# Kernel optimization log

Hardware: AMD Instinct MI355X
Metric: run time of the kernel (lower is better)

The kernel has to match this reference:

```python
import jax, jax.numpy as jnp
import numpy as np

N, E, D, DFF, OUT = 50000, 800000, 128, 256, 119
NUM_MASK = 7500

def setup_inputs() -> dict:
    key = jax.random.key(0)
    ks = jax.random.split(key, 12)
    return {
        "x": jax.random.normal(ks[0], (N, D), jnp.float32),
        "edge_index": jax.random.randint(ks[1], (2, E), 0, N, jnp.int64),
        "edge_attr": jax.random.randint(ks[2], (E, 2), 0, 3, jnp.int64),
        "masked_idx": jax.random.randint(ks[3], (NUM_MASK,), 0, N, jnp.int64),
        "prelu_a": jnp.float32(0.25),
        "W_enc": jax.random.normal(ks[4], (D, D), jnp.float32) * (1.0 / np.sqrt(D)),
        "emb1": jax.random.normal(ks[5], (6, D), jnp.float32) * 0.1,
        "emb2": jax.random.normal(ks[6], (3, D), jnp.float32) * 0.1,
        "W1": jax.random.normal(ks[7], (DFF, D), jnp.float32) * (1.0 / np.sqrt(D)),
        "b1": jnp.zeros((DFF,), jnp.float32),
        "W2": jax.random.normal(ks[8], (OUT, DFF), jnp.float32) * (1.0 / np.sqrt(DFF)),
        "b2": jnp.zeros((OUT,), jnp.float32),
    }

def reference(x, edge_index, edge_attr, masked_idx, prelu_a, W_enc, emb1, emb2, W1, b1, W2, b2):
    n = x.shape[0]
    # PReLU -> enc_to_dec (no bias) -> zero masked nodes
    h = jnp.where(x > 0, x, prelu_a * x)
    h = h @ W_enc.T
    h = h.at[masked_idx].set(0.0)
    # add self loops (self-loop edge_attr = [4, 0])
    loop = jnp.arange(n, dtype=edge_index.dtype)
    src = jnp.concatenate([edge_index[0], loop])
    dst = jnp.concatenate([edge_index[1], loop])
    et = jnp.concatenate([edge_attr[:, 0], jnp.full((n,), 4, edge_attr.dtype)])
    ed = jnp.concatenate([edge_attr[:, 1], jnp.zeros((n,), edge_attr.dtype)])
    edge_emb = emb1[et] + emb2[ed]          # [E+N, D]
    msg = h[src] + edge_emb                 # gather + add
    aggr = jax.ops.segment_sum(msg, dst, num_segments=n)  # scatter-add
    # GIN MLP update
    hid = jax.nn.relu(aggr @ W1.T + b1)
    return hid @ W2.T + b2
```

## Files before the change

### kernel.cpp

```cpp
#include <hip/hip_runtime.h>
#include <hip/hip_fp16.h>


typedef unsigned long long ull;
typedef _Float16 half8 __attribute__((ext_vector_type(8)));
typedef float    f32x4 __attribute__((ext_vector_type(4)));

#define MFMA16(a, b, c) __builtin_amdgcn_mfma_f32_16x16x32_f16(a, b, c, 0, 0, 0)
#define BCAP 4608
#define EPB  2048

__global__ __launch_bounds__(256) void k_wconv(const float* __restrict__ Wen,
                                               const float* __restrict__ W1,
                                               const float* __restrict__ W2,
                                               __half* __restrict__ Wen16,
                                               __half* __restrict__ W1_16,
                                               __half* __restrict__ W2_16p,
                                               int* __restrict__ gcur)
{
    int i = blockIdx.x * 256 + threadIdx.x;
    if (blockIdx.x == 0) gcur[threadIdx.x] = 0;
    if (i < 128 * 128) Wen16[i] = __float2half(Wen[i]);
    if (i < 256 * 128) W1_16[i] = __float2half(W1[i]);
    if (i < 128 * 256) {
        int r = i >> 8;
        W2_16p[i] = (r < 119) ? __float2half(W2[i]) : __half(0.0f);
    }
}

__device__ __forceinline__ half8 prelu_h8(const float* __restrict__ p, float a)
{
    float4 v0 = *(const float4*)p;
    float4 v1 = *(const float4*)(p + 4);
    half8 r;
    r[0] = (_Float16)(v0.x > 0.f ? v0.x : a * v0.x);
    r[1] = (_Float16)(v0.y > 0.f ? v0.y : a * v0.y);
    r[2] = (_Float16)(v0.z > 0.f ? v0.z : a * v0.z);
    r[3] = (_Float16)(v0.w > 0.f ? v0.w : a * v0.w);
    r[4] = (_Float16)(v1.x > 0.f ? v1.x : a * v1.x);
    r[5] = (_Float16)(v1.y > 0.f ? v1.y : a * v1.y);
    r[6] = (_Float16)(v1.z > 0.f ? v1.z : a * v1.z);
    r[7] = (_Float16)(v1.w > 0.f ? v1.w : a * v1.w);
    return r;
}

__global__ __launch_bounds__(256) void k_pre(const float* __restrict__ x,
                                             const __half* __restrict__ Wen16,
                                             const float* __restrict__ prelu_a,
                                             __half* __restrict__ h16,
                                             const int* __restrict__ ei,
                                             const int* __restrict__ ea,
                                             int* __restrict__ gcur,
                                             unsigned int* __restrict__ binned,
                                             int n, int E, int nbEnc, int nbBin)
{
    __shared__ __half Wel[128 * 136];
    __shared__ int lcnt[256];
    int t = threadIdx.x;

    if ((int)blockIdx.x >= nbEnc) {
        int b = blockIdx.x - nbEnc;
        int e0 = b * EPB;
        lcnt[t] = 0;
        __syncthreads();
        unsigned int rec[8];
        int bk[8];
#pragma unroll
        for (int u = 0; u < 8; ++u) {
            int e = e0 + u * 256 + t;
            if (e < E) {
                int src = ei[e];
                int dst = ei[E + e];
                int et  = ea[2 * e];
                int ed  = ea[2 * e + 1];
                rec[u] = (unsigned int)src | ((unsigned int)et << 17)
                       | ((unsigned int)ed << 19)
                       | ((unsigned int)(dst & 255) << 21);
                bk[u] = dst >> 8;
                atomicAdd(&lcnt[bk[u]], 1);
            } else bk[u] = -1;
        }
        __syncthreads();
        int c = lcnt[t];
        lcnt[t] = (c > 0) ? atomicAdd(&gcur[t], c) : 0;
        __syncthreads();
#pragma unroll
        for (int u = 0; u < 8; ++u) {
            if (bk[u] >= 0) {
                int pos = atomicAdd(&lcnt[bk[u]], 1);
                if (pos < BCAP) binned[(size_t)bk[u] * BCAP + pos] = rec[u];
            }
        }
        return;
    }

    for (int c = t; c < 2048; c += 256) {
        int row = c >> 4, slot = c & 15;
        *(uint4*)((char*)Wel + row * 272 + slot * 16) =
            *(const uint4*)((const char*)Wen16 + (size_t)c * 16);
    }
    __syncthreads();
    int lane = t & 63, wid = t >> 6;
    int rowbase = blockIdx.x * 128 + wid * 32;
    int mr0 = min(rowbase + (lane & 15), n - 1);
    int mr1 = min(rowbase + 16 + (lane & 15), n - 1);
    int kg = (lane >> 4) * 8, slotb = lane >> 4;
    float a = prelu_a[0];
    f32x4 acc[16] = {};
#pragma unroll
    for (int ks = 0; ks < 4; ++ks) {
        half8 a0 = prelu_h8(x + ((size_t)mr0 << 7) + ks * 32 + kg, a);
        half8 a1 = prelu_h8(x + ((size_t)mr1 << 7) + ks * 32 + kg, a);
        const char* wp = (const char*)Wel + (size_t)(lane & 15) * 272
                       + (ks * 4 + slotb) * 16;
#pragma unroll
        for (int ct = 0; ct < 8; ++ct) {
            half8 bf = *(const half8*)(wp + ct * (16 * 272));
            acc[ct * 2]     = MFMA16(a0, bf, acc[ct * 2]);
            acc[ct * 2 + 1] = MFMA16(a1, bf, acc[ct * 2 + 1]);
        }
    }
#pragma unroll
    for (int ct = 0; ct < 8; ++ct)
#pragma unroll
        for (int h = 0; h < 2; ++h)
#pragma unroll
            for (int r = 0; r < 4; ++r) {
                int node = rowbase + h * 16 + ((lane >> 4) << 2) + r;
                if (node < n)
                    h16[((size_t)node << 7) + (ct << 4) + (lane & 15)] =
                        __float2half(acc[ct * 2 + h][r]);
            }
}

__global__ void k_mask(const int* __restrict__ midx,
                       unsigned int* __restrict__ h16u, int nm)
{
    int idx = blockIdx.x * blockDim.x + threadIdx.x;
    if (idx >= nm * 64) return;
    int m = idx >> 6, l = idx & 63;
    h16u[(((size_t)midx[m]) << 6) + l] = 0u;
}

__global__ __launch_bounds__(256) void k_bucket(const unsigned int* __restrict__ binned,
                                                const int* __restrict__ gcur,
                                                ull* __restrict__ cnt64,
                                                int* __restrict__ off,
                                                int* __restrict__ sorted,
                                                int n, int nb)
{
    __shared__ ull lc[256];
    __shared__ int sg[2][256];
    __shared__ int curs[256];
    int b = blockIdx.x, t = threadIdx.x;

    int gv = (t < nb) ? min(gcur[t], BCAP) : 0;
    sg[0][t] = gv;
    lc[t] = 0;
    __syncthreads();
    int cb = 0;
    for (int d = 1; d < 256; d <<= 1) {
        int v = sg[cb][t];
        if (t >= d) v += sg[cb][t - d];
        sg[cb ^ 1][t] = v;
        cb ^= 1;
        __syncthreads();
    }
    int ebase = (b == 0) ? 0 : sg[cb][b - 1];
    int mcnt = min(gcur[b], BCAP);
    __syncthreads();

    const unsigned int* bp = binned + (size_t)b * BCAP;
    for (int i = t; i < mcnt; i += 256) {
        unsigned int rec = bp[i];
        int dl = (rec >> 21) & 255;
        int et = (rec >> 17) & 3;
        int ed = (rec >> 19) & 3;
        atomicAdd(&lc[dl], (1ULL << (10 * et)) | (1ULL << (30 + 10 * ed)));
    }
    __syncthreads();

    ull c = lc[t];
    int deg = (int)((c & 1023) + ((c >> 10) & 1023) + ((c >> 20) & 1023));
    sg[0][t] = deg;
    __syncthreads();
    cb = 0;
    for (int d = 1; d < 256; d <<= 1) {
        int v = sg[cb][t];
        if (t >= d) v += sg[cb][t - d];
        sg[cb ^ 1][t] = v;
        cb ^= 1;
        __syncthreads();
    }
    int loc = sg[cb][t] - deg;
    int dst = (b << 8) + t;
    if (dst < n) {
        cnt64[dst] = c;
        off[dst]   = ebase + loc;
    }
    curs[t] = ebase + loc;
    __syncthreads();

    for (int i = t; i < mcnt; i += 256) {
        unsigned int rec = bp[i];
        int dl = (rec >> 21) & 255;
        int p = atomicAdd(&curs[dl], 1);
        sorted[p] = (int)(rec & 0x1FFFF);
    }
}

__global__ __launch_bounds__(256) void k_agg(const unsigned int* __restrict__ h16u,
                                             const int* __restrict__ off,
                                             const ull* __restrict__ cnt64,
                                             const int* __restrict__ sorted,
                                             const float* __restrict__ emb1,
                                             const float* __restrict__ emb2,
                                             unsigned int* __restrict__ aggr16u,
                                             int n)
{
    int lane = threadIdx.x & 63;
    int node = blockIdx.x * 4 + (threadIdx.x >> 6);
    if (node >= n) return;
    int p = lane << 1;
    float2 e10 = *(const float2*)(emb1 + 0 * 128 + p);
    float2 e11 = *(const float2*)(emb1 + 1 * 128 + p);
    float2 e12 = *(const float2*)(emb1 + 2 * 128 + p);
    float2 e14 = *(const float2*)(emb1 + 4 * 128 + p);
    float2 e20 = *(const float2*)(emb2 + 0 * 128 + p);
    float2 e21 = *(const float2*)(emb2 + 1 * 128 + p);
    float2 e22 = *(const float2*)(emb2 + 2 * 128 + p);

    ull c = cnt64[node];
    float c0 = (float)(c & 1023), c1 = (float)((c >> 10) & 1023),
          c2 = (float)((c >> 20) & 1023);
    float d0 = (float)((c >> 30) & 1023), d1 = (float)((c >> 40) & 1023),
          d2 = (float)((c >> 50) & 1023);
    int deg = (int)(c & 1023) + (int)((c >> 10) & 1023) + (int)((c >> 20) & 1023);

    unsigned int hv = h16u[(((size_t)node) << 6) + lane];
    float2 hf = __half22float2(*(__half2*)&hv);
    float2 acc, s1, s2, s3;
    s1 = s2 = s3 = make_float2(0.f, 0.f);
    acc.x = hf.x + e14.x + e20.x;
    acc.y = hf.y + e14.y + e20.y;
    acc.x = fmaf(c0, e10.x, fmaf(c1, e11.x, fmaf(c2, e12.x, acc.x)));
    acc.y = fmaf(c0, e10.y, fmaf(c1, e11.y, fmaf(c2, e12.y, acc.y)));
    acc.x = fmaf(d0, e20.x, fmaf(d1, e21.x, fmaf(d2, e22.x, acc.x)));
    acc.y = fmaf(d0, e20.y, fmaf(d1, e21.y, fmaf(d2, e22.y, acc.y)));

    int i = off[node], e = i + deg;
    for (; i + 3 < e; i += 4) {
        int a0 = sorted[i],     a1 = sorted[i + 1];
        int a2 = sorted[i + 2], a3 = sorted[i + 3];
        unsigned int v0 = h16u[(((size_t)a0) << 6) + lane];
        unsigned int v1 = h16u[(((size_t)a1) << 6) + lane];
        unsigned int v2 = h16u[(((size_t)a2) << 6) + lane];
        unsigned int v3 = h16u[(((size_t)a3) << 6) + lane];
        float2 f0 = __half22float2(*(__half2*)&v0);
        float2 f1 = __half22float2(*(__half2*)&v1);
        float2 f2 = __half22float2(*(__half2*)&v2);
        float2 f3 = __half22float2(*(__half2*)&v3);
        acc.x += f0.x; acc.y += f0.y;
        s1.x  += f1.x; s1.y  += f1.y;
        s2.x  += f2.x; s2.y  += f2.y;
        s3.x  += f3.x; s3.y  += f3.y;
    }
    for (; i < e; ++i) {
        unsigned int v0 = h16u[(((size_t)sorted[i]) << 6) + lane];
        float2 f0 = __half22float2(*(__half2*)&v0);
        acc.x += f0.x; acc.y += f0.y;
    }
    acc.x += s1.x + s2.x + s3.x;
    acc.y += s1.y + s2.y + s3.y;
    __half2 o = __floats2half2_rn(acc.x, acc.y);
    aggr16u[(size_t)node * 64 + lane] = *(unsigned int*)&o;
}

__global__ __launch_bounds__(256, 2) void k_mlp1(const __half* __restrict__ aggr16,
                                                 const __half* __restrict__ W1_16,
                                                 const float* __restrict__ b1,
                                                 __half* __restrict__ hid16, int n)
{
    __shared__ __half Wl[256 * 136];
    int t = threadIdx.x;
    for (int c = t; c < 4096; c += 256) {
        int row = c >> 4, slot = c & 15;
        *(uint4*)((char*)Wl + row * 272 + slot * 16) =
            *(const uint4*)((const char*)W1_16 + (size_t)c * 16);
    }
    __syncthreads();
    int lane = t & 63, wid = t >> 6;
    int rowbase = blockIdx.x * 128 + wid * 32;
    int mr0 = min(rowbase + (lane & 15), n - 1);
    int mr1 = min(rowbase + 16 + (lane & 15), n - 1);
    int kg = (lane >> 4) * 8, slotb = lane >> 4;
    f32x4 acc[32] = {};
#pragma unroll
    for (int ks = 0; ks < 4; ++ks) {
        half8 a0 = *(const half8*)(aggr16 + ((size_t)mr0 << 7) + ks * 32 + kg);
        half8 a1 = *(const half8*)(aggr16 + ((size_t)mr1 << 7) + ks * 32 + kg);
        const char* wp = (const char*)Wl + (size_t)(lane & 15) * 272
                       + (ks * 4 + slotb) * 16;
#pragma unroll
        for (int ct = 0; ct < 16; ++ct) {
            half8 bf = *(const half8*)(wp + ct * (16 * 272));
            acc[ct * 2]     = MFMA16(a0, bf, acc[ct * 2]);
            acc[ct * 2 + 1] = MFMA16(a1, bf, acc[ct * 2 + 1]);
        }
    }
#pragma unroll
    for (int ct = 0; ct < 16; ++ct) {
        int col = (ct << 4) + (lane & 15);
        float bb = b1[col];
#pragma unroll
        for (int h = 0; h < 2; ++h)
#pragma unroll
            for (int r = 0; r < 4; ++r) {
                int node = rowbase + h * 16 + ((lane >> 4) << 2) + r;
                if (node < n) {
                    float v = acc[ct * 2 + h][r] + bb;
                    hid16[((size_t)node << 8) + col] =
                        __float2half(v > 0.f ? v : 0.f);
                }
            }
    }
}

__global__ __launch_bounds__(256) void k_mlp2(const __half* __restrict__ hid16,
                                              const __half* __restrict__ W2_16p,
                                              const float* __restrict__ b2,
                                              float* __restrict__ out, int n)
{
    __shared__ __half W2l[128 * 264];
    int t = threadIdx.x;
    for (int c = t; c < 4096; c += 256) {
        int row = c >> 5, slot = c & 31;
        *(uint4*)((char*)W2l + row * 528 + slot * 16) =
            *(const uint4*)((const char*)W2_16p + (size_t)c * 16);
    }
    __syncthreads();
    int lane = t & 63, wid = t >> 6;
    int rowbase = blockIdx.x * 128 + wid * 32;
    int mr0 = min(rowbase + (lane & 15), n - 1);
    int mr1 = min(rowbase + 16 + (lane & 15), n - 1);
    int kg = (lane >> 4) * 8, slotb = lane >> 4;
    f32x4 acc[16] = {};
#pragma unroll
    for (int ks = 0; ks < 8; ++ks) {
        half8 a0 = *(const half8*)(hid16 + ((size_t)mr0 << 8) + ks * 32 + kg);
        half8 a1 = *(const half8*)(hid16 + ((size_t)mr1 << 8) + ks * 32 + kg);
        const char* wp = (const char*)W2l + (size_t)(lane & 15) * 528
                       + (ks * 4 + slotb) * 16;
#pragma unroll
        for (int ct = 0; ct < 8; ++ct) {
            half8 bf = *(const half8*)(wp + ct * (16 * 528));
            acc[ct * 2]     = MFMA16(a0, bf, acc[ct * 2]);
            acc[ct * 2 + 1] = MFMA16(a1, bf, acc[ct * 2 + 1]);
        }
    }
#pragma unroll
    for (int ct = 0; ct < 8; ++ct) {
        int col = (ct << 4) + (lane & 15);
        if (col >= 119) continue;
        float bb = b2[col];
#pragma unroll
        for (int h = 0; h < 2; ++h)
#pragma unroll
            for (int r = 0; r < 4; ++r) {
                int node = rowbase + h * 16 + ((lane >> 4) << 2) + r;
                if (node < n)
                    out[(size_t)node * 119 + col] = acc[ct * 2 + h][r] + bb;
            }
    }
}

extern "C" void kernel_launch(void* const* d_in, const int* in_sizes, int n_in,
                              void* d_out, int out_size, void* d_ws, size_t ws_size,
                              hipStream_t stream)
{
    const float* x    = (const float*)d_in[0];
    const int*   ei   = (const int*)d_in[1];
    const int*   ea   = (const int*)d_in[2];
    const int*   midx = (const int*)d_in[3];
    const float* pa   = (const float*)d_in[4];
    const float* Wen  = (const float*)d_in[5];
    const float* emb1 = (const float*)d_in[6];
    const float* emb2 = (const float*)d_in[7];
    const float* W1   = (const float*)d_in[8];
    const float* b1   = (const float*)d_in[9];
    const float* W2   = (const float*)d_in[10];
    const float* b2   = (const float*)d_in[11];
    float* out = (float*)d_out;

    int n  = in_sizes[0] / 128;
    int E  = in_sizes[1] / 2;
    int nm = in_sizes[3];
    int nb = (n + 255) >> 8;

    char* ws = (char*)d_ws;
    size_t HB = (size_t)n * 128 * 2;
    __half* aggr16 = (__half*)ws;
    __half* h16    = (__half*)(ws + HB);
    __half* hid16  = (__half*)(ws + 2 * HB);
    char* p = ws + 4 * HB;
    __half* Wen16  = (__half*)p;  p += 128 * 128 * 2;
    __half* W1_16  = (__half*)p;  p += 256 * 128 * 2;
    __half* W2_16p = (__half*)p;  p += 128 * 256 * 2;
    ull* cnt64  = (ull*)p;        p += (size_t)n * 8;
    int* gcur   = (int*)p;        p += 256 * 4;
    int* off    = (int*)p;        p += (size_t)n * 4;
    int* sorted = (int*)p;        p += (size_t)E * 4;
    unsigned int* binned = (unsigned int*)p;
    p += (size_t)nb * BCAP * 4;

    int nbEnc = (n + 127) / 128;
    int nbBin = (E + EPB - 1) / EPB;

    k_wconv<<<128, 256, 0, stream>>>(Wen, W1, W2, Wen16, W1_16, W2_16p, gcur);
    k_pre  <<<nbEnc + nbBin, 256, 0, stream>>>(x, Wen16, pa, h16, ei, ea,
                                               gcur, binned, n, E, nbEnc, nbBin);
    k_mask <<<(nm * 64 + 255) / 256, 256, 0, stream>>>(midx, (unsigned int*)h16, nm);
    k_bucket<<<nb, 256, 0, stream>>>(binned, gcur, cnt64, off, sorted, n, nb);
    k_agg  <<<(n + 3) / 4, 256, 0, stream>>>((const unsigned int*)h16, off, cnt64,
                                             sorted, emb1, emb2,
                                             (unsigned int*)aggr16, n);
    k_mlp1 <<<(n + 127) / 128, 256, 0, stream>>>(aggr16, W1_16, b1, hid16, n);
    k_mlp2 <<<(n + 127) / 128, 256, 0, stream>>>(hid16, W2_16p, b2, out, n);
}
```

Before: 132.1 us.

## Split bucket blocks in halves, widen agg gathers, accumulate neighbors in fp16

The bucket kernel now launches two blocks per bucket, and each block scatters only the destinations in its half of the 256-node range. This doubles parallelism in the sort-scatter phase, though both blocks repeat the scans and the counting pass. The aggregation kernel now gives each node 32 lanes, each loading 8 bytes instead of 4, so the gather memory ops are wider. Neighbor sums are kept in packed fp16 (__hadd2) instead of fp32, which cuts conversion and add instructions but costs accuracy for high-degree nodes.

```diff
diff --git a/kernel.cpp b/kernel.cpp
--- a/kernel.cpp
+++ b/kernel.cpp
@@ -152,7 +152,8 @@
     __shared__ ull lc[256];
     __shared__ int sg[2][256];
     __shared__ int curs[256];
-    int b = blockIdx.x, t = threadIdx.x;
+    int b = blockIdx.x >> 1, half = blockIdx.x & 1;
+    int t = threadIdx.x;
 
     int gv = (t < nb) ? min(gcur[t], BCAP) : 0;
     sg[0][t] = gv;
@@ -194,7 +195,7 @@
     }
     int loc = sg[cb][t] - deg;
     int dst = (b << 8) + t;
-    if (dst < n) {
+    if (dst < n && (t >> 7) == half) {
         cnt64[dst] = c;
         off[dst]   = ebase + loc;
     }
@@ -204,31 +205,33 @@
     for (int i = t; i < mcnt; i += 256) {
         unsigned int rec = bp[i];
         int dl = (rec >> 21) & 255;
+        if ((dl >> 7) != half) continue;
         int p = atomicAdd(&curs[dl], 1);
         sorted[p] = (int)(rec & 0x1FFFF);
     }
 }
 
-__global__ __launch_bounds__(256) void k_agg(const unsigned int* __restrict__ h16u,
+__global__ __launch_bounds__(256) void k_agg(const uint2* __restrict__ h16u2,
                                              const int* __restrict__ off,
                                              const ull* __restrict__ cnt64,
                                              const int* __restrict__ sorted,
                                              const float* __restrict__ emb1,
                                              const float* __restrict__ emb2,
-                                             unsigned int* __restrict__ aggr16u,
+                                             uint2* __restrict__ aggr16u2,
                                              int n)
 {
-    int lane = threadIdx.x & 63;
-    int node = blockIdx.x * 4 + (threadIdx.x >> 6);
+    int t = threadIdx.x;
+    int l32 = t & 31;
+    int node = blockIdx.x * 8 + (t >> 5);
     if (node >= n) return;
-    int p = lane << 1;
-    float2 e10 = *(const float2*)(emb1 + 0 * 128 + p);
-    float2 e11 = *(const float2*)(emb1 + 1 * 128 + p);
-    float2 e12 = *(const float2*)(emb1 + 2 * 128 + p);
-    float2 e14 = *(const float2*)(emb1 + 4 * 128 + p);
-    float2 e20 = *(const float2*)(emb2 + 0 * 128 + p);
-    float2 e21 = *(const float2*)(emb2 + 1 * 128 + p);
-    float2 e22 = *(const float2*)(emb2 + 2 * 128 + p);
+    int p = l32 << 2;
+    float4 E10 = *(const float4*)(emb1 + 0 * 128 + p);
+    float4 E11 = *(const float4*)(emb1 + 1 * 128 + p);
+    float4 E12 = *(const float4*)(emb1 + 2 * 128 + p);
+    float4 E14 = *(const float4*)(emb1 + 4 * 128 + p);
+    float4 E20 = *(const float4*)(emb2 + 0 * 128 + p);
+    float4 E21 = *(const float4*)(emb2 + 1 * 128 + p);
+    float4 E22 = *(const float4*)(emb2 + 2 * 128 + p);
 
     ull c = cnt64[node];
     float c0 = (float)(c & 1023), c1 = (float)((c >> 10) & 1023),
@@ -237,43 +240,61 @@
           d2 = (float)((c >> 50) & 1023);
     int deg = (int)(c & 1023) + (int)((c >> 10) & 1023) + (int)((c >> 20) & 1023);
 
-    unsigned int hv = h16u[(((size_t)node) << 6) + lane];
-    float2 hf = __half22float2(*(__half2*)&hv);
-    float2 acc, s1, s2, s3;
-    s1 = s2 = s3 = make_float2(0.f, 0.f);
-    acc.x = hf.x + e14.x + e20.x;
-    acc.y = hf.y + e14.y + e20.y;
-    acc.x = fmaf(c0, e10.x, fmaf(c1, e11.x, fmaf(c2, e12.x, acc.x)));
-    acc.y = fmaf(c0, e10.y, fmaf(c1, e11.y, fmaf(c2, e12.y, acc.y)));
-    acc.x = fmaf(d0, e20.x, fmaf(d1, e21.x, fmaf(d2, e22.x, acc.x)));
-    acc.y = fmaf(d0, e20.y, fmaf(d1, e21.y, fmaf(d2, e22.y, acc.y)));
-
+    uint2 hv = h16u2[(size_t)node * 32 + l32];
+    float2 hA = __half22float2(*(__half2*)&hv.x);
+    float2 hB = __half22float2(*(__half2*)&hv.y);
+    float4 base;
+    base.x = hA.x + E14.x + E20.x;
+    base.y = hA.y + E14.y + E20.y;
+    base.z = hB.x + E14.z + E20.z;
+    base.w = hB.y + E14.w + E20.w;
+    base.x = fmaf(c0, E10.x, fmaf(c1, E11.x, fmaf(c2, E12.x, base.x)));
+    base.y = fmaf(c0, E10.y, fmaf(c1, E11.y, fmaf(c2, E12.y, base.y)));
+    base.z = fmaf(c0, E10.z, fmaf(c1, E11.z, fmaf(c2, E12.z, base.z)));
+    base.w = fmaf(c0, E10.w, fmaf(c1, E11.w, fmaf(c2, E12.w, base.w)));
+    base.x = fmaf(d0, E20.x, fmaf(d1, E21.x, fmaf(d2, E22.x, base.x)));
+    base.y = fmaf(d0, E20.y, fmaf(d1, E21.y, fmaf(d2, E22.y, base.y)));
+    base.z = fmaf(d0, E20.z, fmaf(d1, E21.z, fmaf(d2, E22.z, base.z)));
+    base.w = fmaf(d0, E20.w, fmaf(d1, E21.w, fmaf(d2, E22.w, base.w)));
+
+    __half2 aL[4], aH[4];
+#pragma unroll
+    for (int u = 0; u < 4; ++u) { aL[u] = __half2(); aH[u] = __half2(); }
     int i = off[node], e = i + deg;
     for (; i + 3 < e; i += 4) {
-        int a0 = sorted[i],     a1 = sorted[i + 1];
-        int a2 = sorted[i + 2], a3 = sorted[i + 3];
-        unsigned int v0 = h16u[(((size_t)a0) << 6) + lane];
-        unsigned int v1 = h16u[(((size_t)a1) << 6) + lane];
-        unsigned int v2 = h16u[(((size_t)a2) << 6) + lane];
-        unsigned int v3 = h16u[(((size_t)a3) << 6) + lane];
-        float2 f0 = __half22float2(*(__half2*)&v0);
-        float2 f1 = __half22float2(*(__half2*)&v1);
-        float2 f2 = __half22float2(*(__half2*)&v2);
-        float2 f3 = __half22float2(*(__half2*)&v3);
-        acc.x += f0.x; acc.y += f0.y;
-        s1.x  += f1.x; s1.y  += f1.y;
-        s2.x  += f2.x; s2.y  += f2.y;
-        s3.x  += f3.x; s3.y  += f3.y;
+        int s0 = sorted[i],     s1 = sorted[i + 1];
+        int s2 = sorted[i + 2], s3 = sorted[i + 3];
+        uint2 v0 = h16u2[(size_t)s0 * 32 + l32];
+        uint2 v1 = h16u2[(size_t)s1 * 32 + l32];
+        uint2 v2 = h16u2[(size_t)s2 * 32 + l32];
+        uint2 v3 = h16u2[(size_t)s3 * 32 + l32];
+        aL[0] = __hadd2(aL[0], *(__half2*)&v0.x);
+        aH[0] = __hadd2(aH[0], *(__half2*)&v0.y);
+        aL[1] = __hadd2(aL[1], *(__half2*)&v1.x);
+        aH[1] = __hadd2(aH[1], *(__half2*)&v1.y);
+        aL[2] = __hadd2(aL[2], *(__half2*)&v2.x);
+        aH[2] = __hadd2(aH[2], *(__half2*)&v2.y);
+        aL[3] = __hadd2(aL[3], *(__half2*)&v3.x);
+        aH[3] = __hadd2(aH[3], *(__half2*)&v3.y);
     }
     for (; i < e; ++i) {
-        unsigned int v0 = h16u[(((size_t)sorted[i]) << 6) + lane];
-        float2 f0 = __half22float2(*(__half2*)&v0);
-        acc.x += f0.x; acc.y += f0.y;
-    }
-    acc.x += s1.x + s2.x + s3.x;
-    acc.y += s1.y + s2.y + s3.y;
-    __half2 o = __floats2half2_rn(acc.x, acc.y);
-    aggr16u[(size_t)node * 64 + lane] = *(unsigned int*)&o;
+        uint2 v0 = h16u2[(size_t)sorted[i] * 32 + l32];
+        aL[0] = __hadd2(aL[0], *(__half2*)&v0.x);
+        aH[0] = __hadd2(aH[0], *(__half2*)&v0.y);
+    }
+#pragma unroll
+    for (int u = 0; u < 4; ++u) {
+        float2 fL = __half22float2(aL[u]);
+        float2 fH = __half22float2(aH[u]);
+        base.x += fL.x; base.y += fL.y;
+        base.z += fH.x; base.w += fH.y;
+    }
+    __half2 oL = __floats2half2_rn(base.x, base.y);
+    __half2 oH = __floats2half2_rn(base.z, base.w);
+    uint2 o;
+    o.x = *(unsigned int*)&oL;
+    o.y = *(unsigned int*)&oH;
+    aggr16u2[(size_t)node * 32 + l32] = o;
 }
 
 __global__ __launch_bounds__(256, 2) void k_mlp1(const __half* __restrict__ aggr16,
@@ -420,10 +441,10 @@
     k_pre  <<<nbEnc + nbBin, 256, 0, stream>>>(x, Wen16, pa, h16, ei, ea,
                                                gcur, binned, n, E, nbEnc, nbBin);
     k_mask <<<(nm * 64 + 255) / 256, 256, 0, stream>>>(midx, (unsigned int*)h16, nm);
-    k_bucket<<<nb, 256, 0, stream>>>(binned, gcur, cnt64, off, sorted, n, nb);
-    k_agg  <<<(n + 3) / 4, 256, 0, stream>>>((const unsigned int*)h16, off, cnt64,
+    k_bucket<<<nb * 2, 256, 0, stream>>>(binned, gcur, cnt64, off, sorted, n, nb);
+    k_agg  <<<(n + 7) / 8, 256, 0, stream>>>((const uint2*)h16, off, cnt64,
                                              sorted, emb1, emb2,
-                                             (unsigned int*)aggr16, n);
+                                             (uint2*)aggr16, n);
     k_mlp1 <<<(n + 127) / 128, 256, 0, stream>>>(aggr16, W1_16, b1, hid16, n);
     k_mlp2 <<<(n + 127) / 128, 256, 0, stream>>>(hid16, W2_16p, b2, out, n);
 }
```

Result: no change. 129.7 us (-1.8%).
